# Kernel optimization log

Measured on AMD Instinct MI355X. Metric: run time of the kernel, lower is better.

Reference implementation:

```python
import jax, jax.numpy as jnp
import numpy as np

N0, N1, N2 = 100000, 25000, 6250
F = 128
OUT = 5


def _mean_agg(feat_src, src, dst, n_dst):
    # DGL copy_u + mean: segment mean over destination nodes (0 for isolated dst)
    s = jax.ops.segment_sum(feat_src[src], dst, num_segments=n_dst)
    cnt = jax.ops.segment_sum(jnp.ones_like(dst, dtype=feat_src.dtype), dst, num_segments=n_dst)
    return s / jnp.maximum(cnt, 1.0)[:, None]


def _graph_conv(feat, src, dst, W, b, n):
    # DGL GraphConv, norm='both': D_src^-1/2 gather-sum D_dst^-1/2, then linear
    dt = feat.dtype
    out_deg = jax.ops.segment_sum(jnp.ones_like(src, dtype=dt), src, num_segments=n)
    in_deg = jax.ops.segment_sum(jnp.ones_like(dst, dtype=dt), dst, num_segments=n)
    ns = jnp.where(out_deg > 0, out_deg ** -0.5, 0.0)
    nd = jnp.where(in_deg > 0, in_deg ** -0.5, 0.0)
    agg = jax.ops.segment_sum((feat * ns[:, None])[src], dst, num_segments=n)
    return (agg * nd[:, None]) @ W + b


def setup_inputs() -> dict:
    key = jax.random.key(0)
    keys = jax.random.split(key, 64)
    _c = iter(range(64))
    def nrm(shape, s=0.05):
        return jax.random.normal(keys[next(_c)], shape, dtype=jnp.float32) * s
    def ri(n, hi):
        return jax.random.randint(keys[next(_c)], (n,), 0, hi)
    inp = {
        'X': nrm((N0, 32), 1.0),
        'g0_src': ri(1600000, N0), 'g0_dst': ri(1600000, N0),
        'g1_src': ri(400000, N1), 'g1_dst': ri(400000, N1),
        'g2_src': ri(100000, N2), 'g2_dst': ri(100000, N2),
        'inc0_src': ri(100000, N0), 'inc0_dst': ri(100000, N1),
        'inc1_src': ri(25000, N1), 'inc1_dst': ri(25000, N2),
        'dec0_src': ri(100000, N2), 'dec0_dst': ri(100000, N1),
        'dec1_src': ri(400000, N1), 'dec1_dst': ri(400000, N0),
        'W_emb': nrm((32, F)), 'b_emb': jnp.zeros((F,), jnp.float32),
        'W_gcn0': nrm((F, F)), 'b_gcn0': jnp.zeros((F,), jnp.float32),
        'W_gcn1': nrm((F, F)), 'b_gcn1': jnp.zeros((F,), jnp.float32),
        'W_gcn2': nrm((F, F)), 'b_gcn2': jnp.zeros((F,), jnp.float32),
        'W_enc0': nrm((F, F)), 'b_enc0': jnp.zeros((F,), jnp.float32),
        'W_enc1': nrm((F, F)), 'b_enc1': jnp.zeros((F,), jnp.float32),
        'W_dec0': nrm((F, F)), 'b_dec0': jnp.zeros((F,), jnp.float32),
        'W_dec1': nrm((F, F)), 'b_dec1': jnp.zeros((F,), jnp.float32),
        'W_head0': nrm((2 * F, OUT)), 'b_head0': jnp.zeros((OUT,), jnp.float32),
        'W_head1': nrm((2 * F, OUT)), 'b_head1': jnp.zeros((OUT,), jnp.float32),
        'W_head2': nrm((2 * F, OUT)), 'b_head2': jnp.zeros((OUT,), jnp.float32),
    }
    return inp


def reference(X, g0_src, g0_dst, g1_src, g1_dst, g2_src, g2_dst,
              inc0_src, inc0_dst, inc1_src, inc1_dst,
              dec0_src, dec0_dst, dec1_src, dec1_dst,
              W_emb, b_emb, W_gcn0, b_gcn0, W_gcn1, b_gcn1, W_gcn2, b_gcn2,
              W_enc0, b_enc0, W_enc1, b_enc1, W_dec0, b_dec0, W_dec1, b_dec1,
              W_head0, b_head0, W_head1, b_head1, W_head2, b_head2):
    # embedding at finest scale
    h0 = X @ W_emb + b_emb                                   # [N0, F]
    # encode + pool fine -> coarse (copy_u/mean)
    h1 = _mean_agg(h0 @ W_enc0 + b_enc0, inc0_src, inc0_dst, N1)   # [N1, F]
    h2 = _mean_agg(h1 @ W_enc1 + b_enc1, inc1_src, inc1_dst, N2)   # [N2, F]
    # intra-scale GraphConv
    g0 = _graph_conv(h0, g0_src, g0_dst, W_gcn0, b_gcn0, N0)
    g1 = _graph_conv(h1, g1_src, g1_dst, W_gcn1, b_gcn1, N1)
    g2 = _graph_conv(h2, g2_src, g2_dst, W_gcn2, b_gcn2, N2)
    # decode coarse -> fine
    d2 = g2
    d1 = _mean_agg(d2 @ W_dec0 + b_dec0, dec0_src, dec0_dst, N1)   # [N1, F]
    d0 = _mean_agg(d1 @ W_dec1 + b_dec1, dec1_src, dec1_dst, N0)   # [N0, F]
    # per-scale heads with softmax
    o0 = jax.nn.softmax(jnp.concatenate([g0, d0], -1) @ W_head0 + b_head0, axis=-1)
    o1 = jax.nn.softmax(jnp.concatenate([g1, d1], -1) @ W_head1 + b_head1, axis=-1)
    o2 = jax.nn.softmax(jnp.concatenate([g2, d2], -1) @ W_head2 + b_head2, axis=-1)
    return jnp.concatenate([o0, o1, o2], axis=0)             # [N0+N1+N2, OUT]
```

## Files before the change

### kernel.cpp

```cpp
#include <hip/hip_runtime.h>

#define F 128
static const int N0 = 100000, N1 = 25000, N2 = 6250;

typedef unsigned short u16;
typedef unsigned int   u32;
typedef __attribute__((ext_vector_type(8))) short bf16x8;
typedef __attribute__((ext_vector_type(4))) float f32x4;

__device__ __forceinline__ float bf2f(u16 u) {
    union { u32 i; float f; } v; v.i = ((u32)u) << 16; return v.f;
}
__device__ __forceinline__ u16 f2bf(float f) {
    u32 u = __float_as_uint(f);
    u += 0x7fff + ((u >> 16) & 1);
    return (u16)(u >> 16);
}

struct Seg7 {
    const int* src[7];
    const int* dst[7];
    int end[7];
    int cbase[7];
    int obase[7];
};
struct W7 { const float* w[7]; };

#define EPT 4
#define CEPT 8
#define SM32  (64*(32+8)*2 + 128*(32+8)*2 + 128*4)


__device__ __forceinline__ void dev_mm32(char* smem, const float* __restrict__ Ap,
                                         const float* __restrict__ W,
                                         const float* __restrict__ bias,
                                         u16* __restrict__ out, int M, int blk) {
    const int K = 32;
    const int KST = K + 8;
    u16* Al = (u16*)smem;
    u16* Wt = (u16*)(smem + 64 * KST * 2);
    float* bl = (float*)(smem + 64 * KST * 2 + 128 * KST * 2);
    int tid = threadIdx.x;
    int m0 = blk * 64;

    for (int i = tid; i < K * 128; i += 256) {
        int k = i >> 7, n = i & 127;
        Wt[n * KST + k] = f2bf(W[i]);
    }
    for (int i = tid; i < 64 * K; i += 256) {
        int r = i / K, c = i % K;
        int gr = m0 + r;
        Al[r * KST + c] = (gr < M) ? f2bf(Ap[(size_t)gr * K + c]) : (u16)0;
    }
    if (tid < 128) bl[tid] = bias[tid];
    __syncthreads();

    int w = tid >> 6, lane = tid & 63, m16 = lane & 15, quad = lane >> 4;
    f32x4 acc[8];
#pragma unroll
    for (int t = 0; t < 8; t++)
#pragma unroll
        for (int r = 0; r < 4; r++) acc[t][r] = 0.f;

    {
        bf16x8 af = *(const bf16x8*)&Al[(w * 16 + m16) * KST + quad * 8];
#pragma unroll
        for (int t = 0; t < 8; t++) {
            bf16x8 bf = *(const bf16x8*)&Wt[(t * 16 + m16) * KST + quad * 8];
            acc[t] = __builtin_amdgcn_mfma_f32_16x16x32_bf16(af, bf, acc[t], 0, 0, 0);
        }
    }
#pragma unroll
    for (int t = 0; t < 8; t++) {
#pragma unroll
        for (int r = 0; r < 4; r++) {
            int gr = m0 + w * 16 + quad * 4 + r;
            if (gr >= M) continue;
            int gc = t * 16 + m16;
            out[(size_t)gr * F + gc] = f2bf(acc[t][r] + bl[gc]);
        }
    }
}

template <bool MASK>
__device__ __forceinline__ void dev_mmd(const u16* __restrict__ Ap,
                                        const u16* __restrict__ Wtg,
                                        const float* __restrict__ bias,
                                        u16* __restrict__ out,
                                        const int* __restrict__ rowptr,
                                        int M, int blk) {
    int tid = threadIdx.x;
    int wv = tid >> 6, lane = tid & 63, m16 = lane & 15, quad = lane >> 4;
    int m0 = blk * 64;
    int arow = m0 + wv * 16 + m16;
    if (arow >= M) arow = M - 1;
    const u16* Arow = Ap + (size_t)arow * F;

    f32x4 acc[8];
#pragma unroll
    for (int t = 0; t < 8; t++)
#pragma unroll
        for (int r = 0; r < 4; r++) acc[t][r] = 0.f;

#pragma unroll
    for (int k0 = 0; k0 < F; k0 += 32) {
        bf16x8 af = *(const bf16x8*)&Arow[k0 + quad * 8];
#pragma unroll
        for (int t = 0; t < 8; t++) {
            bf16x8 bf = *(const bf16x8*)&Wtg[(t * 16 + m16) * F + k0 + quad * 8];
            acc[t] = __builtin_amdgcn_mfma_f32_16x16x32_bf16(af, bf, acc[t], 0, 0, 0);
        }
    }
#pragma unroll
    for (int t = 0; t < 8; t++) {
#pragma unroll
        for (int r = 0; r < 4; r++) {
            int gr = m0 + wv * 16 + quad * 4 + r;
            if (gr >= M) continue;
            int gc = t * 16 + m16;
            bool zrow = false;
            if (MASK) zrow = (rowptr[gr + 1] == rowptr[gr]);
            float v = acc[t][r] + bias[gc];
            out[(size_t)gr * F + gc] = zrow ? (u16)0 : f2bf(v);
        }
    }
}

template <int MODE>
__device__ __forceinline__ void dev_gather(const u16* __restrict__ feat,
                                           const int* __restrict__ rowptr,
                                           const int* __restrict__ col,
                                           const int* __restrict__ od,
                                           u16* __restrict__ out, int M, int blk) {
    int wv = (blk * 256 + (int)threadIdx.x) >> 6;
    if (wv >= M) return;
    int lane = threadIdx.x & 63;
    int fo = lane << 1;
    int beg = rowptr[wv], end = rowptr[wv + 1];
    float a0 = 0.f, a1 = 0.f;
    int j = beg;
    for (; j + 8 <= end; j += 8) {
        int cc[8];
#pragma unroll
        for (int t = 0; t < 8; t++) cc[t] = col[j + t];
        float ss[8];
#pragma unroll
        for (int t = 0; t < 8; t++) {
            if (MODE == 1) { int o = od[cc[t]]; ss[t] = o > 0 ? rsqrtf((float)o) : 0.f; }
            else ss[t] = 1.f;
        }
        ushort2 uu[8];
#pragma unroll
        for (int t = 0; t < 8; t++) uu[t] = *(const ushort2*)&feat[(size_t)cc[t] * F + fo];
#pragma unroll
        for (int t = 0; t < 8; t++) { a0 += bf2f(uu[t].x) * ss[t]; a1 += bf2f(uu[t].y) * ss[t]; }
    }
    for (; j < end; j++) {
        int c = col[j];
        float s = 1.f;
        if (MODE == 1) { int o = od[c]; s = o > 0 ? rsqrtf((float)o) : 0.f; }
        ushort2 u = *(const ushort2*)&feat[(size_t)c * F + fo];
        a0 += bf2f(u.x) * s; a1 += bf2f(u.y) * s;
    }
    int deg = end - beg;
    float fs = (MODE == 0) ? (deg > 0 ? 1.f / (float)deg : 0.f)
                           : (deg > 0 ? rsqrtf((float)deg) : 0.f);
    ushort2 o; o.x = f2bf(a0 * fs); o.y = f2bf(a1 * fs);
    *(ushort2*)&out[(size_t)wv * F + fo] = o;
}

template <bool GD>
__device__ __forceinline__ void dev_head(char* smem, const u16* __restrict__ g,
                                         const u16* __restrict__ d,
                                         const int* __restrict__ rowptr,
                                         const int* __restrict__ col,
                                         const float* __restrict__ Wh,
                                         const float* __restrict__ bh,
                                         float* __restrict__ out, int M, int blk) {
    float* Wl = (float*)smem;
    float* bl = (float*)(smem + 1280 * 4);
    int tid = threadIdx.x;
    for (int i = tid; i < 1280; i += 256) Wl[i] = Wh[i];
    if (tid < 5) bl[tid] = bh[tid];
    __syncthreads();

    int lane = tid & 63;
    int wv = tid >> 6;
    int r0 = blk * 32 + wv * 8;
    int k0 = lane << 1;
    for (int i = 0; i < 8; i++) {
        int row = r0 + i;
        if (row < M) {
            float d0v, d1v;
            if (GD) {
                int beg = rowptr[row], end = rowptr[row + 1];
                d0v = 0.f; d1v = 0.f;
                int j = beg;
                for (; j + 4 <= end; j += 4) {
                    int c0 = col[j], c1 = col[j + 1], c2 = col[j + 2], c3 = col[j + 3];
                    ushort2 u0 = *(const ushort2*)&d[(size_t)c0 * F + k0];
                    ushort2 u1 = *(const ushort2*)&d[(size_t)c1 * F + k0];
                    ushort2 u2 = *(const ushort2*)&d[(size_t)c2 * F + k0];
                    ushort2 u3 = *(const ushort2*)&d[(size_t)c3 * F + k0];
                    d0v += bf2f(u0.x) + bf2f(u1.x) + bf2f(u2.x) + bf2f(u3.x);
                    d1v += bf2f(u0.y) + bf2f(u1.y) + bf2f(u2.y) + bf2f(u3.y);
                }
                for (; j < end; j++) {
                    int c = col[j];
                    ushort2 u = *(const ushort2*)&d[(size_t)c * F + k0];
                    d0v += bf2f(u.x); d1v += bf2f(u.y);
                }
                int deg = end - beg;
                float fs = deg > 0 ? 1.f / (float)deg : 0.f;
                d0v *= fs; d1v *= fs;
            } else {
                ushort2 du = *(const ushort2*)&d[(size_t)row * F + k0];
                d0v = bf2f(du.x); d1v = bf2f(du.y);
            }
            ushort2 gu = *(const ushort2*)&g[(size_t)row * F + k0];
            float g0v = bf2f(gu.x), g1v = bf2f(gu.y);
            float p[5];
#pragma unroll
            for (int o = 0; o < 5; o++) {
                p[o] = g0v * Wl[k0 * 5 + o] + g1v * Wl[(k0 + 1) * 5 + o] +
                       d0v * Wl[(k0 + 128) * 5 + o] + d1v * Wl[(k0 + 129) * 5 + o];
            }
#pragma unroll
            for (int o = 0; o < 5; o++) {
                float v = p[o];
                v += __shfl_xor(v, 32, 64);
                v += __shfl_xor(v, 16, 64);
                v += __shfl_xor(v, 8, 64);
                v += __shfl_xor(v, 4, 64);
                v += __shfl_xor(v, 2, 64);
                v += __shfl_xor(v, 1, 64);
                p[o] = v + bl[o];
            }
            if (lane == 0) {
                float m = p[0];
#pragma unroll
                for (int o = 1; o < 5; o++) m = fmaxf(m, p[o]);
                float e[5], s = 0.f;
#pragma unroll
                for (int o = 0; o < 5; o++) { e[o] = expf(p[o] - m); s += e[o]; }
                float inv = 1.f / s;
#pragma unroll
                for (int o = 0; o < 5; o++) out[(size_t)row * 5 + o] = e[o] * inv;
            }
        }
    }
}


__global__ __launch_bounds__(256) void k_count_emb(Seg7 S, W7 Wsrc,
                                                   u16* __restrict__ WtAll,
                                                   int* __restrict__ cnt,
                                                   u16* __restrict__ occ, int ETOT,
                                                   const float* __restrict__ X,
                                                   const float* __restrict__ Wemb,
                                                   const float* __restrict__ bemb,
                                                   u16* __restrict__ h0,
                                                   int nbMM, int nbPrep) {
    __shared__ char smem[SM32];
    int blk = blockIdx.x;
    if (blk < nbMM) {
        dev_mm32(smem, X, Wemb, bemb, h0, N0, blk);
        return;
    }
    if (blk < nbMM + nbPrep) {
        int g = (blk - nbMM) * 256 + threadIdx.x;
        int m = g >> 14, idx = g & 16383;
        int n = idx >> 7, k = idx & 127;
        WtAll[g] = f2bf(Wsrc.w[m][k * 128 + n]);
        return;
    }
    int base = (blk - nbMM - nbPrep) * (256 * CEPT) + threadIdx.x;
    int ee[CEPT], grow[CEPT];
#pragma unroll
    for (int t = 0; t < CEPT; t++) {
        int e = base + t * 256;
        ee[t] = e;
        grow[t] = -1;
        if (e < ETOT) {
            int s = 0;
            while (e >= S.end[s]) s++;
            int le = e - ((s == 0) ? 0 : S.end[s - 1]);
            grow[t] = S.cbase[s] + S.dst[s][le];
        }
    }
    u32 r[CEPT];
#pragma unroll
    for (int t = 0; t < CEPT; t++)
        if (grow[t] >= 0) r[t] = atomicAdd((u32*)&cnt[grow[t]], 1u);
#pragma unroll
    for (int t = 0; t < CEPT; t++)
        if (grow[t] >= 0) occ[ee[t]] = (u16)r[t];
}

__global__ __launch_bounds__(256) void k_fill_od(Seg7 S,
                                                 const int* __restrict__ rowptr,
                                                 const u16* __restrict__ occ,
                                                 int* __restrict__ col,
                                                 int* __restrict__ od, int ETOT,
                                                 float invRow, float invOd) {
    int win = blockIdx.x & 7;
    int base = ((int)blockIdx.x >> 3) * (256 * EPT) + threadIdx.x;
#pragma unroll
    for (int t = 0; t < EPT; t++) {
        int e = base + t * 256;
        if (e >= ETOT) break;
        int s = 0;
        while (e >= S.end[s]) s++;
        int le = e - ((s == 0) ? 0 : S.end[s - 1]);
        int grow = S.cbase[s] + S.dst[s][le];
        int w1 = (int)((float)grow * invRow); w1 = w1 > 7 ? 7 : w1;
        int sv = -1;
        if (w1 == win || S.obase[s] >= 0) sv = S.src[s][le];
        if (w1 == win) col[rowptr[grow] + (int)occ[e]] = sv;
        if (S.obase[s] >= 0) {
            int gs = S.obase[s] + sv;
            int w2 = (int)((float)gs * invOd); w2 = w2 > 7 ? 7 : w2;
            if (w2 == win) atomicAdd(&od[gs], 1);
        }
    }
}

#define SCHUNK 4096
__global__ __launch_bounds__(1024) void k_scan1(const int* __restrict__ cnt,
                                                int* __restrict__ partial, int n) {
    __shared__ int red[1024];
    int tid = threadIdx.x;
    int base = blockIdx.x * SCHUNK + tid * 4;
    int s = 0;
#pragma unroll
    for (int j = 0; j < 4; j++) { int i = base + j; if (i < n) s += cnt[i]; }
    red[tid] = s;
    __syncthreads();
    for (int d = 512; d > 0; d >>= 1) {
        if (tid < d) red[tid] += red[tid + d];
        __syncthreads();
    }
    if (tid == 0) partial[blockIdx.x] = red[0];
}

__global__ __launch_bounds__(128) void k_scan2(int* __restrict__ partial, int G) {
    __shared__ int sh[128];
    int tid = threadIdx.x;
    sh[tid] = (tid < G) ? partial[tid] : 0;
    __syncthreads();
    for (int d = 1; d < 128; d <<= 1) {
        int t = (tid >= d) ? sh[tid - d] : 0;
        __syncthreads();
        sh[tid] += t;
        __syncthreads();
    }
    if (tid < G) partial[tid] = (tid > 0) ? sh[tid - 1] : 0;
    if (tid == 127) partial[G] = sh[127];
}

__global__ __launch_bounds__(1024) void k_scan3(const int* __restrict__ cnt,
                                                const int* __restrict__ partial,
                                                int* __restrict__ rowptr,
                                                int n, int G) {
    __shared__ int red[1024];
    int tid = threadIdx.x;
    int base = blockIdx.x * SCHUNK + tid * 4;
    int v0 = 0, v1 = 0, v2 = 0, v3 = 0;
    if (base + 0 < n) v0 = cnt[base + 0];
    if (base + 1 < n) v1 = cnt[base + 1];
    if (base + 2 < n) v2 = cnt[base + 2];
    if (base + 3 < n) v3 = cnt[base + 3];
    red[tid] = v0 + v1 + v2 + v3;
    __syncthreads();
    for (int d = 1; d < 1024; d <<= 1) {
        int t = (tid >= d) ? red[tid - d] : 0;
        __syncthreads();
        red[tid] += t;
        __syncthreads();
    }
    int off = partial[blockIdx.x] + ((tid > 0) ? red[tid - 1] : 0);
    if (base + 0 < n) { rowptr[base + 0] = off; off += v0; }
    if (base + 1 < n) { rowptr[base + 1] = off; off += v1; }
    if (base + 2 < n) { rowptr[base + 2] = off; off += v2; }
    if (base + 3 < n) { rowptr[base + 3] = off; off += v3; }
    if (blockIdx.x == 0 && tid == 0) rowptr[n] = partial[G];
}

template <int MODE>
__global__ __launch_bounds__(256) void k_gather(const u16* __restrict__ feat,
                                                const int* __restrict__ rowptr,
                                                const int* __restrict__ col,
                                                const int* __restrict__ od,
                                                u16* __restrict__ out, int M) {
    dev_gather<MODE>(feat, rowptr, col, od, out, M, blockIdx.x);
}

template <int MA, int MB>
__global__ __launch_bounds__(256) void k_gather2(
    const u16* fA, const int* rpA, const int* oA, u16* outA, int MAr, int nbA,
    const u16* fB, const int* rpB, const int* oB, u16* outB, int MBr,
    const int* __restrict__ col) {
    if ((int)blockIdx.x < nbA) dev_gather<MA>(fA, rpA, col, oA, outA, MAr, blockIdx.x);
    else                       dev_gather<MB>(fB, rpB, col, oB, outB, MBr, blockIdx.x - nbA);
}

template <bool MASK>
__global__ __launch_bounds__(256) void k_mmd(const u16* __restrict__ Ap,
                                             const u16* __restrict__ Wtg,
                                             const float* __restrict__ bias,
                                             u16* __restrict__ out,
                                             const int* __restrict__ rowptr, int M) {
    dev_mmd<MASK>(Ap, Wtg, bias, out, rowptr, M, blockIdx.x);
}

__global__ __launch_bounds__(256) void k_mmd2(
    const u16* A1, const u16* Wt1, const float* b1, u16* o1, const int* rp1, int M1, int nb1,
    const u16* A2, const u16* Wt2, const float* b2, u16* o2, int M2) {
    if ((int)blockIdx.x < nb1) dev_mmd<true >(A1, Wt1, b1, o1, rp1, M1, blockIdx.x);
    else                       dev_mmd<false>(A2, Wt2, b2, o2, nullptr, M2, blockIdx.x - nb1);
}

__global__ __launch_bounds__(256) void k_head3(
    const u16* Ga, const u16* dFeat, const int* rpD1, const int* colp,
    const float* Wa, const float* Ba, int nb0,
    const u16* Gb, const u16* Db, const float* Wb, const float* Bb, int nb1,
    const u16* Gc, const float* Wc, const float* Bc,
    float* __restrict__ out) {
    __shared__ char smem[1280 * 4 + 32];
    int b = blockIdx.x;
    if (b < nb0)            dev_head<true >(smem, Ga, dFeat, rpD1, colp, Wa, Ba, out, N0, b);
    else if (b < nb0 + nb1) dev_head<false>(smem, Gb, Db, nullptr, nullptr, Wb, Bb, out + (size_t)N0 * 5, N1, b - nb0);
    else                    dev_head<false>(smem, Gc, Gc, nullptr, nullptr, Wc, Bc, out + (size_t)(N0 + N1) * 5, N2, b - nb0 - nb1);
}

extern "C" void kernel_launch(void* const* d_in, const int* in_sizes, int n_in,
                              void* d_out, int out_size, void* d_ws, size_t ws_size,
                              hipStream_t stream) {
    const float* X = (const float*)d_in[0];
    const int *g0s = (const int*)d_in[1], *g0d = (const int*)d_in[2];
    const int *g1s = (const int*)d_in[3], *g1d = (const int*)d_in[4];
    const int *g2s = (const int*)d_in[5], *g2d = (const int*)d_in[6];
    const int *i0s = (const int*)d_in[7], *i0d = (const int*)d_in[8];
    const int *i1s = (const int*)d_in[9], *i1d = (const int*)d_in[10];
    const int *dc0s = (const int*)d_in[11], *dc0d = (const int*)d_in[12];
    const int *dc1s = (const int*)d_in[13], *dc1d = (const int*)d_in[14];
    const float *Wemb = (const float*)d_in[15], *bemb = (const float*)d_in[16];
    const float *Wg0 = (const float*)d_in[17], *bg0 = (const float*)d_in[18];
    const float *Wg1 = (const float*)d_in[19], *bg1 = (const float*)d_in[20];
    const float *Wg2 = (const float*)d_in[21], *bg2 = (const float*)d_in[22];
    const float *We0 = (const float*)d_in[23], *be0 = (const float*)d_in[24];
    const float *We1 = (const float*)d_in[25], *be1 = (const float*)d_in[26];
    const float *Wd0 = (const float*)d_in[27], *bd0 = (const float*)d_in[28];
    const float *Wd1 = (const float*)d_in[29], *bd1 = (const float*)d_in[30];
    const float *Wh0 = (const float*)d_in[31], *bh0 = (const float*)d_in[32];
    const float *Wh1 = (const float*)d_in[33], *bh1 = (const float*)d_in[34];
    const float *Wh2 = (const float*)d_in[35], *bh2 = (const float*)d_in[36];
    const int Eg0 = in_sizes[1], Eg1 = in_sizes[3], Eg2 = in_sizes[5];
    const int Ei0 = in_sizes[7], Ei1 = in_sizes[9];
    const int Ed0 = in_sizes[11], Ed1 = in_sizes[13];
    (void)n_in; (void)out_size; (void)ws_size;

    const int B_I0 = 0;
    const int B_I1 = B_I0 + N1;
    const int B_G2 = B_I1 + N2;
    const int B_D0 = B_G2 + N2;
    const int B_G1 = B_D0 + N1;
    const int B_G0 = B_G1 + N1;
    const int B_D1 = B_G0 + N0;
    const int NROWS = B_D1 + N0;
    const int ETOT  = Eg0 + Eg1 + Eg2 + Ei0 + Ei1 + Ed0 + Ed1;
    const int OB_G0 = 0, OB_G1 = N0, OB_G2 = N0 + N1;
    const int NOD = N0 + N1 + N2;
    const int G = (NROWS + SCHUNK - 1) / SCHUNK;
    const int rowsPerWin = (NROWS + 7) / 8;
    const int odPerWin   = (NOD + 7) / 8;
    const float invRow = 1.0f / (float)rowsPerWin;
    const float invOd  = 1.0f / (float)odPerWin;
    const int NCH = (ETOT + 256 * EPT - 1) / (256 * EPT);

    char* wsb = (char*)d_ws;
    size_t off = 0;
    auto alloc = [&](size_t bytes) -> char* {
        char* p = wsb + off;
        off = (off + bytes + 255) & ~(size_t)255;
        return p;
    };
    u16* h0  = (u16*)alloc((size_t)N0 * F * 2);
    u16* h1  = (u16*)alloc((size_t)N1 * F * 2);
    u16* h2  = (u16*)alloc((size_t)N2 * F * 2);
    u16* G0  = (u16*)alloc((size_t)N0 * F * 2);
    u16* G1  = (u16*)alloc((size_t)N1 * F * 2);
    u16* G2  = (u16*)alloc((size_t)N2 * F * 2);
    u16* D1  = (u16*)alloc((size_t)N1 * F * 2);
    u16* agg = (u16*)alloc((size_t)N0 * F * 2);
    u16* bN1 = (u16*)alloc((size_t)N1 * F * 2);
    u16* bN2 = (u16*)alloc((size_t)N2 * F * 2);
    u16* pA  = D1;
    u16* WtAll = (u16*)alloc((size_t)7 * 16384 * 2);
    int* cnt    = (int*)alloc((size_t)NROWS * 4);
    int* od     = (int*)alloc((size_t)NOD * 4);
    int* rowptr = (int*)alloc((size_t)(NROWS + 1) * 4);
    u16* occ    = (u16*)alloc((size_t)ETOT * 2);
    int* col    = (int*)alloc((size_t)ETOT * 4);
    int* part   = (int*)alloc((size_t)(G + 1) * 4);
    float* out = (float*)d_out;

    u16* WtE0 = WtAll + 0 * 16384;
    u16* WtG0 = WtAll + 1 * 16384;
    u16* WtE1 = WtAll + 2 * 16384;
    u16* WtG1 = WtAll + 3 * 16384;
    u16* WtG2 = WtAll + 4 * 16384;
    u16* WtD0 = WtAll + 5 * 16384;
    u16* WtD1 = WtAll + 6 * 16384;
    W7 Wsrc;
    Wsrc.w[0] = We0; Wsrc.w[1] = Wg0; Wsrc.w[2] = We1; Wsrc.w[3] = Wg1;
    Wsrc.w[4] = Wg2; Wsrc.w[5] = Wd0; Wsrc.w[6] = Wd1;

    Seg7 S;
    S.src[0] = i0s;  S.dst[0] = i0d;  S.cbase[0] = B_I0; S.obase[0] = -1;
    S.src[1] = i1s;  S.dst[1] = i1d;  S.cbase[1] = B_I1; S.obase[1] = -1;
    S.src[2] = g2s;  S.dst[2] = g2d;  S.cbase[2] = B_G2; S.obase[2] = OB_G2;
    S.src[3] = dc0s; S.dst[3] = dc0d; S.cbase[3] = B_D0; S.obase[3] = -1;
    S.src[4] = g1s;  S.dst[4] = g1d;  S.cbase[4] = B_G1; S.obase[4] = OB_G1;
    S.src[5] = g0s;  S.dst[5] = g0d;  S.cbase[5] = B_G0; S.obase[5] = OB_G0;
    S.src[6] = dc1s; S.dst[6] = dc1d; S.cbase[6] = B_D1; S.obase[6] = -1;
    {
        int Es[7] = {Ei0, Ei1, Eg2, Ed0, Eg1, Eg0, Ed1};
        int acc = 0;
        for (int i = 0; i < 7; i++) { acc += Es[i]; S.end[i] = acc; }
    }

    const int nbEmb   = (N0 + 63) / 64;
    const int nbPrep  = (7 * 16384) / 256;
    const int nbCount = (ETOT + 256 * CEPT - 1) / (256 * CEPT);
    const int nbFill  = NCH * 8;

    hipMemsetAsync(cnt, 0, (size_t)((char*)od - (char*)cnt) + (size_t)NOD * 4, stream);
    k_count_emb<<<nbEmb + nbPrep + nbCount, 256, 0, stream>>>(
        S, Wsrc, WtAll, cnt, occ, ETOT, X, Wemb, bemb, h0, nbEmb, nbPrep);
    k_scan1<<<G, 1024, 0, stream>>>(cnt, part, NROWS);
    k_scan2<<<1, 128, 0, stream>>>(part, G);
    k_scan3<<<G, 1024, 0, stream>>>(cnt, part, rowptr, NROWS, G);
    k_fill_od<<<nbFill, 256, 0, stream>>>(S, rowptr, occ, col, od, ETOT, invRow, invOd);

    {
        int nbA = (N1 + 3) / 4, nbB = (N0 + 3) / 4;
        k_gather2<0, 1><<<nbA + nbB, 256, 0, stream>>>(
            h0, rowptr + B_I0, nullptr, pA, N1, nbA,
            h0, rowptr + B_G0, od + OB_G0, agg, N0, col);
    }
    {
        int nb1 = (N1 + 63) / 64, nb2 = (N0 + 63) / 64;
        k_mmd2<<<nb1 + nb2, 256, 0, stream>>>(pA, WtE0, be0, h1, rowptr + B_I0, N1, nb1,
                                              agg, WtG0, bg0, G0, N0);
    }
    {
        int nbA = (N2 + 3) / 4, nbB = (N1 + 3) / 4;
        k_gather2<0, 1><<<nbA + nbB, 256, 0, stream>>>(
            h1, rowptr + B_I1, nullptr, bN2, N2, nbA,
            h1, rowptr + B_G1, od + OB_G1, bN1, N1, col);
    }
    {
        int nb1 = (N2 + 63) / 64, nb2 = (N1 + 63) / 64;
        k_mmd2<<<nb1 + nb2, 256, 0, stream>>>(bN2, WtE1, be1, h2, rowptr + B_I1, N2, nb1,
                                              bN1, WtG1, bg1, G1, N1);
    }
    k_gather<1><<<(N2 + 3) / 4, 256, 0, stream>>>(h2, rowptr + B_G2, col, od + OB_G2, bN2, N2);
    k_mmd<false><<<(N2 + 63) / 64, 256, 0, stream>>>(bN2, WtG2, bg2, G2, nullptr, N2);
    k_mmd<false><<<(N2 + 63) / 64, 256, 0, stream>>>(G2, WtD0, bd0, bN2, nullptr, N2);
    k_gather<0><<<(N1 + 3) / 4, 256, 0, stream>>>(bN2, rowptr + B_D0, col, nullptr, D1, N1);
    k_mmd<false><<<(N1 + 63) / 64, 256, 0, stream>>>(D1, WtD1, bd1, bN1, nullptr, N1);
    {
        int nb0 = (N0 + 31) / 32, nb1 = (N1 + 31) / 32, nb2 = (N2 + 31) / 32;
        k_head3<<<nb0 + nb1 + nb2, 256, 0, stream>>>(G0, bN1, rowptr + B_D1, col, Wh0, bh0, nb0,
                                                     G1, D1, Wh1, bh1, nb1,
                                                     G2, Wh2, bh2, out);
    }
}
```

Measured before the change: 691.9 us.

## Use half-wave 8-byte gathers and regroup gather/matmul kernel fusion schedule

Gather and head kernels now assign 32 lanes per row, each loading 4 bf16 values (8 bytes) instead of 64 lanes loading 2. This widens the loads and doubles the rows in flight per wave. The launch schedule is also regrouped. The pooling gather for level 1 runs alone first, then the enc0 matmul is fused with the large g0 GraphConv gather, and the g0 matmul is deferred and fused with the level-2 gather. The aim is to overlap independent work and raise memory-level parallelism, at the cost of an extra launch and different load balance.

```diff
diff --git a/kernel.cpp b/kernel.cpp
--- a/kernel.cpp
+++ b/kernel.cpp
@@ -127,17 +127,17 @@
 }
 
 template <int MODE>
-__device__ __forceinline__ void dev_gather(const u16* __restrict__ feat,
-                                           const int* __restrict__ rowptr,
-                                           const int* __restrict__ col,
-                                           const int* __restrict__ od,
-                                           u16* __restrict__ out, int M, int blk) {
-    int wv = (blk * 256 + (int)threadIdx.x) >> 6;
-    if (wv >= M) return;
-    int lane = threadIdx.x & 63;
-    int fo = lane << 1;
-    int beg = rowptr[wv], end = rowptr[wv + 1];
-    float a0 = 0.f, a1 = 0.f;
+__device__ __forceinline__ void dev_gather32(const u16* __restrict__ feat,
+                                             const int* __restrict__ rowptr,
+                                             const int* __restrict__ col,
+                                             const int* __restrict__ od,
+                                             u16* __restrict__ out, int M, int blk) {
+    int row = (blk * 256 + (int)threadIdx.x) >> 5;
+    if (row >= M) return;
+    int l32 = threadIdx.x & 31;
+    int fo = l32 << 2;
+    int beg = rowptr[row], end = rowptr[row + 1];
+    float a0 = 0.f, a1 = 0.f, a2 = 0.f, a3 = 0.f;
     int j = beg;
     for (; j + 8 <= end; j += 8) {
         int cc[8];
@@ -149,24 +149,30 @@
             if (MODE == 1) { int o = od[cc[t]]; ss[t] = o > 0 ? rsqrtf((float)o) : 0.f; }
             else ss[t] = 1.f;
         }
-        ushort2 uu[8];
-#pragma unroll
-        for (int t = 0; t < 8; t++) uu[t] = *(const ushort2*)&feat[(size_t)cc[t] * F + fo];
-#pragma unroll
-        for (int t = 0; t < 8; t++) { a0 += bf2f(uu[t].x) * ss[t]; a1 += bf2f(uu[t].y) * ss[t]; }
+        ushort4 uu[8];
+#pragma unroll
+        for (int t = 0; t < 8; t++) uu[t] = *(const ushort4*)&feat[(size_t)cc[t] * F + fo];
+#pragma unroll
+        for (int t = 0; t < 8; t++) {
+            a0 += bf2f(uu[t].x) * ss[t]; a1 += bf2f(uu[t].y) * ss[t];
+            a2 += bf2f(uu[t].z) * ss[t]; a3 += bf2f(uu[t].w) * ss[t];
+        }
     }
     for (; j < end; j++) {
         int c = col[j];
         float s = 1.f;
         if (MODE == 1) { int o = od[c]; s = o > 0 ? rsqrtf((float)o) : 0.f; }
-        ushort2 u = *(const ushort2*)&feat[(size_t)c * F + fo];
+        ushort4 u = *(const ushort4*)&feat[(size_t)c * F + fo];
         a0 += bf2f(u.x) * s; a1 += bf2f(u.y) * s;
+        a2 += bf2f(u.z) * s; a3 += bf2f(u.w) * s;
     }
     int deg = end - beg;
     float fs = (MODE == 0) ? (deg > 0 ? 1.f / (float)deg : 0.f)
                            : (deg > 0 ? rsqrtf((float)deg) : 0.f);
-    ushort2 o; o.x = f2bf(a0 * fs); o.y = f2bf(a1 * fs);
-    *(ushort2*)&out[(size_t)wv * F + fo] = o;
+    ushort4 o;
+    o.x = f2bf(a0 * fs); o.y = f2bf(a1 * fs);
+    o.z = f2bf(a2 * fs); o.w = f2bf(a3 * fs);
+    *(ushort4*)&out[(size_t)row * F + fo] = o;
 }
 
 template <bool GD>
@@ -184,51 +190,57 @@
     if (tid < 5) bl[tid] = bh[tid];
     __syncthreads();
 
-    int lane = tid & 63;
-    int wv = tid >> 6;
-    int r0 = blk * 32 + wv * 8;
-    int k0 = lane << 1;
-    for (int i = 0; i < 8; i++) {
-        int row = r0 + i;
+    int grp = tid >> 5;
+    int l32 = tid & 31;
+    int k0 = l32 << 2;
+    for (int i = 0; i < 4; i++) {
+        int row = blk * 32 + grp * 4 + i;
         if (row < M) {
-            float d0v, d1v;
+            float dv[4];
             if (GD) {
                 int beg = rowptr[row], end = rowptr[row + 1];
-                d0v = 0.f; d1v = 0.f;
+                dv[0] = dv[1] = dv[2] = dv[3] = 0.f;
                 int j = beg;
                 for (; j + 4 <= end; j += 4) {
                     int c0 = col[j], c1 = col[j + 1], c2 = col[j + 2], c3 = col[j + 3];
-                    ushort2 u0 = *(const ushort2*)&d[(size_t)c0 * F + k0];
-                    ushort2 u1 = *(const ushort2*)&d[(size_t)c1 * F + k0];
-                    ushort2 u2 = *(const ushort2*)&d[(size_t)c2 * F + k0];
-                    ushort2 u3 = *(const ushort2*)&d[(size_t)c3 * F + k0];
-                    d0v += bf2f(u0.x) + bf2f(u1.x) + bf2f(u2.x) + bf2f(u3.x);
-                    d1v += bf2f(u0.y) + bf2f(u1.y) + bf2f(u2.y) + bf2f(u3.y);
+                    ushort4 u0 = *(const ushort4*)&d[(size_t)c0 * F + k0];
+                    ushort4 u1 = *(const ushort4*)&d[(size_t)c1 * F + k0];
+                    ushort4 u2 = *(const ushort4*)&d[(size_t)c2 * F + k0];
+                    ushort4 u3 = *(const ushort4*)&d[(size_t)c3 * F + k0];
+                    dv[0] += bf2f(u0.x) + bf2f(u1.x) + bf2f(u2.x) + bf2f(u3.x);
+                    dv[1] += bf2f(u0.y) + bf2f(u1.y) + bf2f(u2.y) + bf2f(u3.y);
+                    dv[2] += bf2f(u0.z) + bf2f(u1.z) + bf2f(u2.z) + bf2f(u3.z);
+                    dv[3] += bf2f(u0.w) + bf2f(u1.w) + bf2f(u2.w) + bf2f(u3.w);
                 }
                 for (; j < end; j++) {
                     int c = col[j];
-                    ushort2 u = *(const ushort2*)&d[(size_t)c * F + k0];
-                    d0v += bf2f(u.x); d1v += bf2f(u.y);
+                    ushort4 u = *(const ushort4*)&d[(size_t)c * F + k0];
+                    dv[0] += bf2f(u.x); dv[1] += bf2f(u.y);
+                    dv[2] += bf2f(u.z); dv[3] += bf2f(u.w);
                 }
                 int deg = end - beg;
                 float fs = deg > 0 ? 1.f / (float)deg : 0.f;
-                d0v *= fs; d1v *= fs;
+#pragma unroll
+                for (int q = 0; q < 4; q++) dv[q] *= fs;
             } else {
-                ushort2 du = *(const ushort2*)&d[(size_t)row * F + k0];
-                d0v = bf2f(du.x); d1v = bf2f(du.y);
+                ushort4 du = *(const ushort4*)&d[(size_t)row * F + k0];
+                dv[0] = bf2f(du.x); dv[1] = bf2f(du.y);
+                dv[2] = bf2f(du.z); dv[3] = bf2f(du.w);
             }
-            ushort2 gu = *(const ushort2*)&g[(size_t)row * F + k0];
-            float g0v = bf2f(gu.x), g1v = bf2f(gu.y);
+            ushort4 gu = *(const ushort4*)&g[(size_t)row * F + k0];
+            float gv[4] = {bf2f(gu.x), bf2f(gu.y), bf2f(gu.z), bf2f(gu.w)};
             float p[5];
 #pragma unroll
             for (int o = 0; o < 5; o++) {
-                p[o] = g0v * Wl[k0 * 5 + o] + g1v * Wl[(k0 + 1) * 5 + o] +
-                       d0v * Wl[(k0 + 128) * 5 + o] + d1v * Wl[(k0 + 129) * 5 + o];
+                float v = 0.f;
+#pragma unroll
+                for (int q = 0; q < 4; q++)
+                    v += gv[q] * Wl[(k0 + q) * 5 + o] + dv[q] * Wl[(k0 + q + 128) * 5 + o];
+                p[o] = v;
             }
 #pragma unroll
             for (int o = 0; o < 5; o++) {
                 float v = p[o];
-                v += __shfl_xor(v, 32, 64);
                 v += __shfl_xor(v, 16, 64);
                 v += __shfl_xor(v, 8, 64);
                 v += __shfl_xor(v, 4, 64);
@@ -236,7 +248,7 @@
                 v += __shfl_xor(v, 1, 64);
                 p[o] = v + bl[o];
             }
-            if (lane == 0) {
+            if (l32 == 0) {
                 float m = p[0];
 #pragma unroll
                 for (int o = 1; o < 5; o++) m = fmaxf(m, p[o]);
@@ -387,21 +399,21 @@
 }
 
 template <int MODE>
-__global__ __launch_bounds__(256) void k_gather(const u16* __restrict__ feat,
-                                                const int* __restrict__ rowptr,
-                                                const int* __restrict__ col,
-                                                const int* __restrict__ od,
-                                                u16* __restrict__ out, int M) {
-    dev_gather<MODE>(feat, rowptr, col, od, out, M, blockIdx.x);
+__global__ __launch_bounds__(256) void k_g32(const u16* __restrict__ feat,
+                                             const int* __restrict__ rowptr,
+                                             const int* __restrict__ col,
+                                             const int* __restrict__ od,
+                                             u16* __restrict__ out, int M) {
+    dev_gather32<MODE>(feat, rowptr, col, od, out, M, blockIdx.x);
 }
 
 template <int MA, int MB>
-__global__ __launch_bounds__(256) void k_gather2(
+__global__ __launch_bounds__(256) void k_g32x2(
     const u16* fA, const int* rpA, const int* oA, u16* outA, int MAr, int nbA,
     const u16* fB, const int* rpB, const int* oB, u16* outB, int MBr,
     const int* __restrict__ col) {
-    if ((int)blockIdx.x < nbA) dev_gather<MA>(fA, rpA, col, oA, outA, MAr, blockIdx.x);
-    else                       dev_gather<MB>(fB, rpB, col, oB, outB, MBr, blockIdx.x - nbA);
+    if ((int)blockIdx.x < nbA) dev_gather32<MA>(fA, rpA, col, oA, outA, MAr, blockIdx.x);
+    else                       dev_gather32<MB>(fB, rpB, col, oB, outB, MBr, blockIdx.x - nbA);
 }
 
 template <bool MASK>
@@ -418,6 +430,22 @@
     const u16* A2, const u16* Wt2, const float* b2, u16* o2, int M2) {
     if ((int)blockIdx.x < nb1) dev_mmd<true >(A1, Wt1, b1, o1, rp1, M1, blockIdx.x);
     else                       dev_mmd<false>(A2, Wt2, b2, o2, nullptr, M2, blockIdx.x - nb1);
+}
+
+__global__ __launch_bounds__(256) void k_mmd_g32(
+    const u16* A1, const u16* Wt1, const float* b1, u16* o1, const int* rp1, int M1, int nb1,
+    const u16* feat, const int* rp2, const int* od2, u16* out2, int M2,
+    const int* __restrict__ col) {
+    if ((int)blockIdx.x < nb1) dev_mmd<true>(A1, Wt1, b1, o1, rp1, M1, blockIdx.x);
+    else dev_gather32<1>(feat, rp2, col, od2, out2, M2, blockIdx.x - nb1);
+}
+
+__global__ __launch_bounds__(256) void k_g32_mmd(
+    const u16* feat, const int* rp1, const int* od1, u16* out1, int M1, int nb1,
+    const u16* A2, const u16* Wt2, const float* b2, u16* o2, int M2,
+    const int* __restrict__ col) {
+    if ((int)blockIdx.x < nb1) dev_gather32<1>(feat, rp1, col, od1, out1, M1, blockIdx.x);
+    else dev_mmd<false>(A2, Wt2, b2, o2, nullptr, M2, blockIdx.x - nb1);
 }
 
 __global__ __launch_bounds__(256) void k_head3(
@@ -543,20 +571,16 @@
     k_scan3<<<G, 1024, 0, stream>>>(cnt, part, rowptr, NROWS, G);
     k_fill_od<<<nbFill, 256, 0, stream>>>(S, rowptr, occ, col, od, ETOT, invRow, invOd);
 
+    k_g32<0><<<(N1 * 32 + 255) / 256, 256, 0, stream>>>(h0, rowptr + B_I0, col, nullptr, pA, N1);
     {
-        int nbA = (N1 + 3) / 4, nbB = (N0 + 3) / 4;
-        k_gather2<0, 1><<<nbA + nbB, 256, 0, stream>>>(
-            h0, rowptr + B_I0, nullptr, pA, N1, nbA,
-            h0, rowptr + B_G0, od + OB_G0, agg, N0, col);
+        int nb1 = (N1 + 63) / 64;
+        int nb2 = (N0 * 32 + 255) / 256;
+        k_mmd_g32<<<nb1 + nb2, 256, 0, stream>>>(pA, WtE0, be0, h1, rowptr + B_I0, N1, nb1,
+                                                 h0, rowptr + B_G0, od + OB_G0, agg, N0, col);
     }
     {
-        int nb1 = (N1 + 63) / 64, nb2 = (N0 + 63) / 64;
-        k_mmd2<<<nb1 + nb2, 256, 0, stream>>>(pA, WtE0, be0, h1, rowptr + B_I0, N1, nb1,
-                                              agg, WtG0, bg0, G0, N0);
-    }
-    {
-        int nbA = (N2 + 3) / 4, nbB = (N1 + 3) / 4;
-        k_gather2<0, 1><<<nbA + nbB, 256, 0, stream>>>(
+        int nbA = (N2 * 32 + 255) / 256, nbB = (N1 * 32 + 255) / 256;
+        k_g32x2<0, 1><<<nbA + nbB, 256, 0, stream>>>(
             h1, rowptr + B_I1, nullptr, bN2, N2, nbA,
             h1, rowptr + B_G1, od + OB_G1, bN1, N1, col);
     }
@@ -565,10 +589,15 @@
         k_mmd2<<<nb1 + nb2, 256, 0, stream>>>(bN2, WtE1, be1, h2, rowptr + B_I1, N2, nb1,
                                               bN1, WtG1, bg1, G1, N1);
     }
-    k_gather<1><<<(N2 + 3) / 4, 256, 0, stream>>>(h2, rowptr + B_G2, col, od + OB_G2, bN2, N2);
+    {
+        int nb1 = (N2 * 32 + 255) / 256;
+        int nb2 = (N0 + 63) / 64;
+        k_g32_mmd<<<nb1 + nb2, 256, 0, stream>>>(h2, rowptr + B_G2, od + OB_G2, bN2, N2, nb1,
+                                                 agg, WtG0, bg0, G0, N0, col);
+    }
     k_mmd<false><<<(N2 + 63) / 64, 256, 0, stream>>>(bN2, WtG2, bg2, G2, nullptr, N2);
     k_mmd<false><<<(N2 + 63) / 64, 256, 0, stream>>>(G2, WtD0, bd0, bN2, nullptr, N2);
-    k_gather<0><<<(N1 + 3) / 4, 256, 0, stream>>>(bN2, rowptr + B_D0, col, nullptr, D1, N1);
+    k_g32<0><<<(N1 * 32 + 255) / 256, 256, 0, stream>>>(bN2, rowptr + B_D0, col, nullptr, D1, N1);
     k_mmd<false><<<(N1 + 63) / 64, 256, 0, stream>>>(D1, WtD1, bd1, bN1, nullptr, N1);
     {
         int nb0 = (N0 + 31) / 32, nb1 = (N1 + 31) / 32, nb2 = (N2 + 31) / 32;
```

New measurement: 680.9 us. Within noise of the previous version (-1.6%).
